# Kernel tuning notes

Hardware: AMD Instinct MI355X
Metric: run time of the kernel (lower is better)

Reference implementation:

```python
import jax, jax.numpy as jnp
import numpy as np

B, NQ, N, D_IN, D_KEY, D_MODEL = 8, 2048, 2048, 512, 512, 512


def setup_inputs() -> dict:
    key = jax.random.key(0)
    k1, k2, k3, k4, k5, k6 = jax.random.split(key, 6)
    lim_k = np.sqrt(6.0 / (D_IN + D_KEY))
    lim_v = np.sqrt(6.0 / (D_IN + D_MODEL))
    return {
        "node_features": jax.random.normal(k1, (B, N, D_IN), dtype=jnp.float32),
        "query": jax.random.normal(k2, (B, NQ, D_IN), dtype=jnp.float32),
        "mask": jax.random.bernoulli(k3, 0.3, (NQ, B, N)),  # True = masked out
        "wq": jax.random.uniform(k4, (D_IN, D_KEY), jnp.float32, -lim_k, lim_k),
        "wk": jax.random.uniform(k5, (D_IN, D_KEY), jnp.float32, -lim_k, lim_k),
        "wv": jax.random.uniform(k6, (D_IN, D_MODEL), jnp.float32, -lim_v, lim_v),
    }


def reference(node_features, query, mask, wq, wk, wv):
    # Projections
    Q = query @ wq              # [B, NQ, d_key]
    K = node_features @ wk      # [B, N, d_key]
    V = node_features @ wv      # [B, N, d_model]
    # Raw scores [B, NQ, N]
    scores = jnp.einsum("bqd,bnd->bqn", Q, K)
    b, nq, n = scores.shape
    # Faithful to tf: reshape to (NQ, B, N), mask with float32.min, reshape back
    s = scores.reshape(nq, b, n)
    masked = jnp.where(mask, jnp.finfo(jnp.float32).min, s).reshape(b, nq, n)
    # Scale AFTER masking (as in the original), then softmax over keys
    attn = jax.nn.softmax(masked / jnp.sqrt(jnp.float32(K.shape[-1])), axis=-1)
    return attn @ V             # [B, NQ, d_model]
```

## Files before the change

kernel.cpp:

```cpp
#include <hip/hip_runtime.h>

typedef __attribute__((ext_vector_type(8))) short bf16x8;
typedef __attribute__((ext_vector_type(4))) float f32x4;

__device__ __forceinline__ unsigned short f2bf(float f) {
  unsigned int u = __builtin_bit_cast(unsigned int, f);
  u += 0x7fffu + ((u >> 16) & 1u);
  return (unsigned short)(u >> 16);
}

#define GLD16(gp, lp) __builtin_amdgcn_global_load_lds( \
    (const __attribute__((address_space(1))) unsigned int*)(gp), \
    (__attribute__((address_space(3))) unsigned int*)(lp), 16, 0, 0)

__global__ __launch_bounds__(256) void pack_mask(
    const unsigned char* __restrict__ m, unsigned long long* __restrict__ pm)
{
  __shared__ int mode1;
  if (threadIdx.x == 0) mode1 = 0;
  __syncthreads();

  const int g = blockIdx.x * 256 + threadIdx.x;
  const size_t base = (size_t)g * 64;

  uint4 v[4];
  const uint4* p1 = (const uint4*)(m + base);
  v[0] = p1[0]; v[1] = p1[1]; v[2] = p1[2]; v[3] = p1[3];
  unsigned int probe = 0;
#pragma unroll
  for (int j = 0; j < 4; ++j)
    probe |= (v[j].x | v[j].y | v[j].z | v[j].w);
  if (probe & 0x0000ff00u) mode1 = 1;
  __syncthreads();

  unsigned long long bits = 0;
  if (mode1) {
#pragma unroll
    for (int j = 0; j < 4; ++j) {
      unsigned int w[4] = {v[j].x, v[j].y, v[j].z, v[j].w};
#pragma unroll
      for (int q = 0; q < 4; ++q) {
        unsigned int u = w[q];
#pragma unroll
        for (int b = 0; b < 4; ++b)
          if ((u >> (8 * b)) & 0xffu) bits |= 1ull << (j * 16 + q * 4 + b);
      }
    }
  } else {
    const uint4* p4 = (const uint4*)(m + base * 4);
#pragma unroll
    for (int j = 0; j < 16; ++j) {
      uint4 w = p4[j];
      if (w.x) bits |= 1ull << (j * 4 + 0);
      if (w.y) bits |= 1ull << (j * 4 + 1);
      if (w.z) bits |= 1ull << (j * 4 + 2);
      if (w.w) bits |= 1ull << (j * 4 + 3);
    }
  }
  pm[g] = bits;
}

__global__ void prep(const float* __restrict__ query, const float* __restrict__ node,
                     const float* __restrict__ wq, const float* __restrict__ wk,
                     const float* __restrict__ wv,
                     unsigned short* __restrict__ Xq, unsigned short* __restrict__ Xn,
                     unsigned short* __restrict__ oq, unsigned short* __restrict__ ok,
                     unsigned short* __restrict__ ov, float* __restrict__ sums)
{
  const int b = blockIdx.x;
  if (b < 16384) {
    int i = b * 256 + threadIdx.x;
    const float* src;
    unsigned short* dst;
    int j;
    if (i < 2097152) { src = query; dst = Xq; j = i; }
    else             { src = node;  dst = Xn; j = i - 2097152; }
    float4 v = ((const float4*)src)[j];
    ushort4 o;
    o.x = f2bf(v.x); o.y = f2bf(v.y); o.z = f2bf(v.z); o.w = f2bf(v.w);
    ((ushort4*)dst)[j] = o;
  } else if (b < 19456) {
    int idx = (b - 16384) * 256 + threadIdx.x;
    int w = idx >> 18;
    int rem = idx & 262143;
    int n = rem >> 9, k = rem & 511;
    const float* W = (w == 0) ? wq : (w == 1) ? wk : wv;
    unsigned short* O = (w == 0) ? oq : (w == 1) ? ok : ov;
    O[n * 512 + k] = f2bf(W[k * 512 + n]);
  } else {
    int idx = (b - 19456) * 256 + threadIdx.x;
    sums[idx] = 0.0f;
  }
}

__device__ __forceinline__ void core128(
    const unsigned short* __restrict__ Ab, const unsigned short* __restrict__ Bb,
    void* __restrict__ Cb, long ldA, long ldB, long ldO, int nk,
    long bm, long bn, char* smem, int mode,
    const unsigned long long* __restrict__ pmask, float* __restrict__ sumz,
    const float* __restrict__ sums_ro)
{
  const int tid = threadIdx.x;
  const int lane = tid & 63;
  const int wid = tid >> 6;
  const int wr = wid >> 1, wc = wid & 1;
  const int fr = lane & 15, fq = lane >> 4;

  const int srow = tid >> 2;
  const int sch = (tid & 3) ^ ((srow >> 1) & 3);

  char* bufs[3] = { smem, smem + 16384, smem + 32768 };

#define STAGE_C(buf, kt) do { \
    const long k0_ = (long)(kt) << 5; \
    GLD16(Ab + (bm + srow) * ldA + k0_ + sch * 8,        (buf) + tid * 16); \
    GLD16(Ab + (bm + 64 + srow) * ldA + k0_ + sch * 8,   (buf) + 4096 + tid * 16); \
    GLD16(Bb + (bn + srow) * ldB + k0_ + sch * 8,        (buf) + 8192 + tid * 16); \
    GLD16(Bb + (bn + 64 + srow) * ldB + k0_ + sch * 8,   (buf) + 12288 + tid * 16); \
  } while (0)

  int aoff[4], boff[4];
#pragma unroll
  for (int i = 0; i < 4; ++i) {
    const int ra = wr * 64 + i * 16 + fr;
    aoff[i] = ra * 64 + (fq ^ ((ra >> 1) & 3)) * 16;
    const int rb = wc * 64 + i * 16 + fr;
    boff[i] = 8192 + rb * 64 + (fq ^ ((rb >> 1) & 3)) * 16;
  }

  f32x4 acc[4][4] = {};

  STAGE_C(bufs[0], 0);
  STAGE_C(bufs[1], 1);
  char* c0 = bufs[0]; char* c1 = bufs[1]; char* c2 = bufs[2];

  for (int t = 0; t < nk; ++t) {
    __builtin_amdgcn_sched_barrier(0);
    __builtin_amdgcn_s_barrier();
    if (t + 2 < nk) {
      STAGE_C(c2, t + 2);
      asm volatile("s_waitcnt vmcnt(8)" ::: "memory");
    } else if (t + 2 == nk) {
      asm volatile("s_waitcnt vmcnt(4)" ::: "memory");
    } else {
      asm volatile("s_waitcnt vmcnt(0)" ::: "memory");
    }
    __builtin_amdgcn_s_barrier();
    __builtin_amdgcn_sched_barrier(0);

    bf16x8 a[4];
#pragma unroll
    for (int mi = 0; mi < 4; ++mi)
      a[mi] = *(const bf16x8*)(c0 + aoff[mi]);
    __builtin_amdgcn_s_setprio(1);
#pragma unroll
    for (int nj = 0; nj < 4; ++nj) {
      const bf16x8 b = *(const bf16x8*)(c0 + boff[nj]);
#pragma unroll
      for (int mi = 0; mi < 4; ++mi)
        acc[mi][nj] = __builtin_amdgcn_mfma_f32_16x16x32_bf16(a[mi], b, acc[mi][nj], 0, 0, 0);
    }
    __builtin_amdgcn_s_setprio(0);

    char* tmp = c0; c0 = c1; c1 = c2; c2 = tmp;
  }
#undef STAGE_C

  const float SCALE = 0.04419417382415922f;
  if (mode == 0) {
    unsigned short* C = (unsigned short*)Cb;
#pragma unroll
    for (int mi = 0; mi < 4; ++mi)
#pragma unroll
      for (int nj = 0; nj < 4; ++nj) {
        const long row = bm + wr * 64 + mi * 16 + fq * 4;
        const long col = bn + wc * 64 + nj * 16 + fr;
#pragma unroll
        for (int r = 0; r < 4; ++r)
          C[(row + r) * ldO + col] = f2bf(acc[mi][nj][r]);
      }
  } else if (mode == 1) {
    unsigned short* C = (unsigned short*)Cb;
    const long wword = (bn >> 6) + wc;
#pragma unroll
    for (int mi = 0; mi < 4; ++mi) {
      const long rowb = bm + wr * 64 + mi * 16 + fq * 4;
#pragma unroll
      for (int r = 0; r < 4; ++r) {
        const long row = rowb + r;
        const unsigned long long w = pmask[row * 32 + wword];
        unsigned short* Crow = C + row * ldO + bn + wc * 64 + fr;
        float s = 0.f;
#pragma unroll
        for (int nj = 0; nj < 4; ++nj) {
          const int sh = nj * 16 + fr;
          float e = ((w >> sh) & 1ull) ? 0.0f : __expf(acc[mi][nj][r] * SCALE);
          s += e;
          Crow[nj * 16] = f2bf(e);
        }
        s += __shfl_xor(s, 1); s += __shfl_xor(s, 2);
        s += __shfl_xor(s, 4); s += __shfl_xor(s, 8);
        if (fr == 0) atomicAdd(&sumz[row], s);
      }
    }
  } else {
    float* C = (float*)Cb;
#pragma unroll
    for (int mi = 0; mi < 4; ++mi) {
      const long rowb = bm + wr * 64 + mi * 16 + fq * 4;
#pragma unroll
      for (int r = 0; r < 4; ++r) {
        const long row = rowb + r;
        const float iv = 1.0f / sums_ro[row];
        const long colb = bn + wc * 64 + fr;
#pragma unroll
        for (int nj = 0; nj < 4; ++nj)
          C[row * ldO + colb + nj * 16] = acc[mi][nj][r] * iv;
      }
    }
  }
}

__global__ __launch_bounds__(256, 3) void gemm_proj(
    const unsigned short* __restrict__ Xq, const unsigned short* __restrict__ Xn,
    const unsigned short* __restrict__ Wqt, const unsigned short* __restrict__ Wkt,
    const unsigned short* __restrict__ Wvt,
    unsigned short* __restrict__ Q, unsigned short* __restrict__ Kb,
    unsigned short* __restrict__ Vt)
{
  extern __shared__ char smem[];
  const int z = blockIdx.z;
  if (z == 0) {
    core128(Xq, Wqt, Q, 512, 512, 512, 16,
            (long)blockIdx.x * 128, (long)blockIdx.y * 128, smem, 0,
            nullptr, nullptr, nullptr);
  } else if (z == 1) {
    core128(Xn, Wkt, Kb, 512, 512, 512, 16,
            (long)blockIdx.x * 128, (long)blockIdx.y * 128, smem, 0,
            nullptr, nullptr, nullptr);
  } else {
    core128(Wvt, Xn, Vt, 512, 512, 16384, 16,
            (long)blockIdx.y * 128, (long)blockIdx.x * 128, smem, 0,
            nullptr, nullptr, nullptr);
  }
}

__global__ __launch_bounds__(256, 3) void gemm_scores(
    const unsigned short* __restrict__ Qg, const unsigned short* __restrict__ Kg,
    unsigned short* __restrict__ Eg, const unsigned long long* __restrict__ pm,
    float* __restrict__ sums)
{
  extern __shared__ char smem[];
  const long z = blockIdx.x;
  core128(Qg + z * 1048576, Kg + z * 1048576, Eg + z * 4194304,
          512, 512, 2048, 16,
          (long)blockIdx.y * 128, (long)blockIdx.z * 128, smem, 1,
          pm + z * 65536, sums + z * 2048, nullptr);
}

__global__ __launch_bounds__(256, 3) void gemm_pv(
    const unsigned short* __restrict__ E, const unsigned short* __restrict__ Vt,
    const float* __restrict__ sums, float* __restrict__ O)
{
  extern __shared__ char smem[];
  const long z = blockIdx.x;
  core128(E + z * 4194304, Vt + z * 2048, O + z * 1048576,
          2048, 16384, 512, 64,
          (long)blockIdx.z * 128, (long)blockIdx.y * 128, smem, 2,
          nullptr, nullptr, sums + z * 2048);
}

extern "C" void kernel_launch(void* const* d_in, const int* in_sizes, int n_in,
                              void* d_out, int out_size, void* d_ws, size_t ws_size,
                              hipStream_t stream) {
  const float* node  = (const float*)d_in[0];
  const float* query = (const float*)d_in[1];
  const unsigned char* mask = (const unsigned char*)d_in[2];
  const float* wq = (const float*)d_in[3];
  const float* wk = (const float*)d_in[4];
  const float* wv = (const float*)d_in[5];
  float* out = (float*)d_out;

  char* ws = (char*)d_ws;
  unsigned short* Q   = (unsigned short*)(ws);
  unsigned short* Kb  = (unsigned short*)(ws + 16777216);
  unsigned short* Vt  = (unsigned short*)(ws + 33554432);
  unsigned short* E   = (unsigned short*)(ws + 50331648);
  unsigned short* Xq  = (unsigned short*)(ws + 50331648);
  unsigned short* Xn  = (unsigned short*)(ws + 50331648 + 16777216);
  unsigned short* Wqt = (unsigned short*)(ws + 50331648 + 33554432);
  unsigned short* Wkt = Wqt + 262144;
  unsigned short* Wvt = Wkt + 262144;
  float* sums = (float*)(ws + 117440512);
  unsigned long long* pm = (unsigned long long*)(ws + 118489088);

  pack_mask<<<2048, 256, 0, stream>>>(mask, pm);
  prep<<<19520, 256, 0, stream>>>(query, node, wq, wk, wv,
                                  Xq, Xn, Wqt, Wkt, Wvt, sums);

  dim3 gp(128, 4, 3);
  gemm_proj<<<gp, 256, 49152, stream>>>(Xq, Xn, Wqt, Wkt, Wvt, Q, Kb, Vt);

  dim3 gs(8, 16, 16);
  gemm_scores<<<gs, 256, 49152, stream>>>(Q, Kb, E, pm, sums);

  dim3 gv(8, 4, 16);
  gemm_pv<<<gv, 256, 49152, stream>>>(E, Vt, sums, out);
}
```

Baseline: 205.1 us.

## Fold Wq·Wkᵀ into one matrix to skip the K projection

Precomputes M = Wq·Wkᵀ (stored transposed) in a small GEMM, then projects the query once as T = Xq·M and scores directly against the bf16 node features, which removes the separate K projection GEMM. The projection kernel now launches two z-slices instead of three. This assumes d_key equals d_in, so the FLOP count is unchanged for the score GEMM. The trade-off is an extra small kernel launch and an extra bf16 rounding of the fused matrix, which may change numerical error.

```diff
diff --git a/kernel.cpp b/kernel.cpp
--- a/kernel.cpp
+++ b/kernel.cpp
@@ -64,8 +64,8 @@
                      const float* __restrict__ wq, const float* __restrict__ wk,
                      const float* __restrict__ wv,
                      unsigned short* __restrict__ Xq, unsigned short* __restrict__ Xn,
-                     unsigned short* __restrict__ oq, unsigned short* __restrict__ ok,
-                     unsigned short* __restrict__ ov, float* __restrict__ sums)
+                     unsigned short* __restrict__ wqb, unsigned short* __restrict__ wkb,
+                     unsigned short* __restrict__ wvt, float* __restrict__ sums)
 {
   const int b = blockIdx.x;
   if (b < 16384) {
@@ -83,10 +83,12 @@
     int idx = (b - 16384) * 256 + threadIdx.x;
     int w = idx >> 18;
     int rem = idx & 262143;
-    int n = rem >> 9, k = rem & 511;
-    const float* W = (w == 0) ? wq : (w == 1) ? wk : wv;
-    unsigned short* O = (w == 0) ? oq : (w == 1) ? ok : ov;
-    O[n * 512 + k] = f2bf(W[k * 512 + n]);
+    if (w == 0)      wqb[rem] = f2bf(wq[rem]);
+    else if (w == 1) wkb[rem] = f2bf(wk[rem]);
+    else {
+      int n = rem >> 9, k = rem & 511;
+      wvt[n * 512 + k] = f2bf(wv[k * 512 + n]);
+    }
   } else {
     int idx = (b - 19456) * 256 + threadIdx.x;
     sums[idx] = 0.0f;
@@ -221,21 +223,24 @@
   }
 }
 
+__global__ __launch_bounds__(256, 3) void gemm_mt(
+    const unsigned short* __restrict__ wkb, const unsigned short* __restrict__ wqb,
+    unsigned short* __restrict__ MT)
+{
+  extern __shared__ char smem[];
+  core128(wkb, wqb, MT, 512, 512, 512, 16,
+          (long)blockIdx.x * 128, (long)blockIdx.y * 128, smem, 0,
+          nullptr, nullptr, nullptr);
+}
+
 __global__ __launch_bounds__(256, 3) void gemm_proj(
     const unsigned short* __restrict__ Xq, const unsigned short* __restrict__ Xn,
-    const unsigned short* __restrict__ Wqt, const unsigned short* __restrict__ Wkt,
-    const unsigned short* __restrict__ Wvt,
-    unsigned short* __restrict__ Q, unsigned short* __restrict__ Kb,
-    unsigned short* __restrict__ Vt)
+    const unsigned short* __restrict__ MT, const unsigned short* __restrict__ Wvt,
+    unsigned short* __restrict__ T, unsigned short* __restrict__ Vt)
 {
   extern __shared__ char smem[];
-  const int z = blockIdx.z;
-  if (z == 0) {
-    core128(Xq, Wqt, Q, 512, 512, 512, 16,
-            (long)blockIdx.x * 128, (long)blockIdx.y * 128, smem, 0,
-            nullptr, nullptr, nullptr);
-  } else if (z == 1) {
-    core128(Xn, Wkt, Kb, 512, 512, 512, 16,
+  if (blockIdx.z == 0) {
+    core128(Xq, MT, T, 512, 512, 512, 16,
             (long)blockIdx.x * 128, (long)blockIdx.y * 128, smem, 0,
             nullptr, nullptr, nullptr);
   } else {
@@ -246,13 +251,13 @@
 }
 
 __global__ __launch_bounds__(256, 3) void gemm_scores(
-    const unsigned short* __restrict__ Qg, const unsigned short* __restrict__ Kg,
+    const unsigned short* __restrict__ T, const unsigned short* __restrict__ Xn,
     unsigned short* __restrict__ Eg, const unsigned long long* __restrict__ pm,
     float* __restrict__ sums)
 {
   extern __shared__ char smem[];
   const long z = blockIdx.x;
-  core128(Qg + z * 1048576, Kg + z * 1048576, Eg + z * 4194304,
+  core128(T + z * 1048576, Xn + z * 1048576, Eg + z * 4194304,
           512, 512, 2048, 16,
           (long)blockIdx.y * 128, (long)blockIdx.z * 128, smem, 1,
           pm + z * 65536, sums + z * 2048, nullptr);
@@ -282,27 +287,29 @@
   float* out = (float*)d_out;
 
   char* ws = (char*)d_ws;
-  unsigned short* Q   = (unsigned short*)(ws);
-  unsigned short* Kb  = (unsigned short*)(ws + 16777216);
+  unsigned short* T   = (unsigned short*)(ws);
+  unsigned short* Xn  = (unsigned short*)(ws + 16777216);
   unsigned short* Vt  = (unsigned short*)(ws + 33554432);
   unsigned short* E   = (unsigned short*)(ws + 50331648);
   unsigned short* Xq  = (unsigned short*)(ws + 50331648);
-  unsigned short* Xn  = (unsigned short*)(ws + 50331648 + 16777216);
-  unsigned short* Wqt = (unsigned short*)(ws + 50331648 + 33554432);
-  unsigned short* Wkt = Wqt + 262144;
-  unsigned short* Wvt = Wkt + 262144;
+  unsigned short* wqb = (unsigned short*)(ws + 67108864);
+  unsigned short* wkb = (unsigned short*)(ws + 67633152);
+  unsigned short* Wvt = (unsigned short*)(ws + 68157440);
+  unsigned short* MT  = (unsigned short*)(ws + 68681728);
   float* sums = (float*)(ws + 117440512);
   unsigned long long* pm = (unsigned long long*)(ws + 118489088);
 
   pack_mask<<<2048, 256, 0, stream>>>(mask, pm);
   prep<<<19520, 256, 0, stream>>>(query, node, wq, wk, wv,
-                                  Xq, Xn, Wqt, Wkt, Wvt, sums);
-
-  dim3 gp(128, 4, 3);
-  gemm_proj<<<gp, 256, 49152, stream>>>(Xq, Xn, Wqt, Wkt, Wvt, Q, Kb, Vt);
+                                  Xq, Xn, wqb, wkb, Wvt, sums);
+
+  gemm_mt<<<dim3(4, 4, 1), 256, 49152, stream>>>(wkb, wqb, MT);
+
+  dim3 gp(128, 4, 2);
+  gemm_proj<<<gp, 256, 49152, stream>>>(Xq, Xn, MT, Wvt, T, Vt);
 
   dim3 gs(8, 16, 16);
-  gemm_scores<<<gs, 256, 49152, stream>>>(Q, Kb, E, pm, sums);
+  gemm_scores<<<gs, 256, 49152, stream>>>(T, Xn, E, pm, sums);
 
   dim3 gv(8, 4, 16);
   gemm_pv<<<gv, 256, 49152, stream>>>(E, Vt, sums, out);
```

New measurement: 201.4 us. Within noise of the previous version (-1.8%).
